# Performance work log

Hardware: AMD Instinct MI355X
Metric: run time of the kernel (lower is better)

## Reference

```python
import jax, jax.numpy as jnp
import numpy as np

N_NODES = 100000
N_EDGES = 640000
H_FEATS = 128


def setup_inputs() -> dict:
    key = jax.random.key(0)
    k_h, k_src, k_dst, k_w1, k_b1, k_w2, k_b2 = jax.random.split(key, 7)
    h = jax.random.normal(k_h, (N_NODES, H_FEATS), dtype=jnp.float32)
    src = jax.random.randint(k_src, (N_EDGES,), 0, N_NODES, dtype=jnp.int64)
    dst = jax.random.randint(k_dst, (N_EDGES,), 0, N_NODES, dtype=jnp.int64)
    # nn.Linear params: W1 (h_feats, 2*h_feats) as (out, in); store transposed for x @ W
    lim1 = 1.0 / np.sqrt(2 * H_FEATS)
    W1 = jax.random.uniform(k_w1, (2 * H_FEATS, H_FEATS), jnp.float32, -lim1, lim1)
    b1 = jax.random.uniform(k_b1, (H_FEATS,), jnp.float32, -lim1, lim1)
    lim2 = 1.0 / np.sqrt(H_FEATS)
    W2 = jax.random.uniform(k_w2, (H_FEATS, 1), jnp.float32, -lim2, lim2)
    b2 = jax.random.uniform(k_b2, (1,), jnp.float32, -lim2, lim2)
    return {"h": h, "src": src, "dst": dst, "W1": W1, "b1": b1, "W2": W2, "b2": b2}


def reference(h, src, dst, W1, b1, W2, b2):
    # gather src/dst node features per edge and concat: [E, 2*h_feats]
    he = jnp.concatenate([h[src], h[dst]], axis=1)
    hidden = jax.nn.relu(he @ W1 + b1)          # [E, h_feats]
    score = (hidden @ W2 + b2)[:, 0]            # [E]
    return score
```

## Files before the change

### kernel.cpp

```cpp
#include <hip/hip_runtime.h>

#define N_NODES 100000
#define N_EDGES 640000
#define F 128

typedef __attribute__((ext_vector_type(8))) short short8;
typedef __attribute__((ext_vector_type(4))) float float4v;

static __device__ __forceinline__ unsigned short f2bf(float f) {
    unsigned int u = __float_as_uint(f);
    u += 0x7fffu + ((u >> 16) & 1u);
    return (unsigned short)(u >> 16);
}

__global__ __launch_bounds__(256) void prep_wt(
    const float* __restrict__ W1, unsigned short* __restrict__ Wt)
{
    int id = blockIdx.x * 256 + threadIdx.x;
    int n = id >> 7, k = id & 127;
    float v = W1[((n & 128) + k) * 128 + (n & 127)];
    Wt[id] = f2bf(v);
}

__global__ __launch_bounds__(256) void node_proj(
    const float* __restrict__ h, const unsigned short* __restrict__ Wt,
    const float* __restrict__ b1,
    unsigned short* __restrict__ A, unsigned short* __restrict__ B)
{
    __shared__ unsigned short h_lds[64 * 136];
    __shared__ unsigned short w_lds[128 * 136];

    const int tid  = threadIdx.x;
    const int y    = blockIdx.y;
    const int node0 = blockIdx.x * 64;

#pragma unroll
    for (int i = 0; i < 8; ++i) {
        int idx = i * 256 + tid;
        int m = idx >> 5, c4 = idx & 31;
        int row_g = node0 + m; if (row_g >= N_NODES) row_g = N_NODES - 1;
        float4 v = *(const float4*)(h + (size_t)row_g * F + c4 * 4);
        uint2 p;
        p.x = (unsigned)f2bf(v.x) | ((unsigned)f2bf(v.y) << 16);
        p.y = (unsigned)f2bf(v.z) | ((unsigned)f2bf(v.w) << 16);
        *(uint2*)&h_lds[m * 136 + c4 * 4] = p;
    }
#pragma unroll
    for (int i = 0; i < 8; ++i) {
        int idx = i * 256 + tid;
        int n = idx >> 4, c = idx & 15;
        uint4 v = *(const uint4*)(Wt + (size_t)(y * 128 + n) * F + c * 8);
        *(uint4*)&w_lds[n * 136 + c * 8] = v;
    }
    __syncthreads();

    const int lane = tid & 63;
    const int l16  = lane & 15;
    const int quad = lane >> 4;
    const int w    = tid >> 6;
    const int n0w  = w * 32;
    const int kq   = quad * 8;

    float4v acc[4][2];
#pragma unroll
    for (int i = 0; i < 4; ++i)
#pragma unroll
        for (int j = 0; j < 2; ++j) acc[i][j] = (float4v){0.f, 0.f, 0.f, 0.f};

#pragma unroll
    for (int k0 = 0; k0 < 128; k0 += 32) {
        short8 af[4], bf[2];
#pragma unroll
        for (int i = 0; i < 4; ++i)
            af[i] = *(const short8*)&h_lds[(i * 16 + l16) * 136 + k0 + kq];
#pragma unroll
        for (int j = 0; j < 2; ++j)
            bf[j] = *(const short8*)&w_lds[(n0w + j * 16 + l16) * 136 + k0 + kq];
#pragma unroll
        for (int i = 0; i < 4; ++i)
#pragma unroll
            for (int j = 0; j < 2; ++j)
                acc[i][j] = __builtin_amdgcn_mfma_f32_16x16x32_bf16(
                    af[i], bf[j], acc[i][j], 0, 0, 0);
    }

    unsigned short* outp = (y == 0) ? A : B;
#pragma unroll
    for (int j = 0; j < 2; ++j) {
        int col = n0w + j * 16 + l16;
        float bias = (y == 0) ? b1[col] : 0.f;
#pragma unroll
        for (int i = 0; i < 4; ++i) {
#pragma unroll
            for (int r = 0; r < 4; ++r) {
                int row_g = node0 + i * 16 + quad * 4 + r;
                if (row_g < N_NODES)
                    outp[(size_t)row_g * F + col] = f2bf(acc[i][j][r] + bias);
            }
        }
    }
}

__global__ __launch_bounds__(256) void edge_score(
    const unsigned short* __restrict__ A, const unsigned short* __restrict__ B,
    const int* __restrict__ src, const int* __restrict__ dst,
    const float* __restrict__ W2, const float* __restrict__ b2,
    float* __restrict__ out)
{
    const int tid = threadIdx.x;
    const int sub = tid & 7;
    const int e   = blockIdx.x * 32 + (tid >> 3);
    const int j0  = sub * 16;

    const int s = src[e];
    const int d = dst[e];
    const uint4* Ap = (const uint4*)(A + (size_t)s * F + j0);
    const uint4* Bp = (const uint4*)(B + (size_t)d * F + j0);
    uint4 a0 = Ap[0], a1 = Ap[1];
    uint4 b0 = Bp[0], b1v = Bp[1];
    const float4* Wp = (const float4*)(W2 + j0);
    float4 w0 = Wp[0], w1 = Wp[1], w2 = Wp[2], w3 = Wp[3];

    float sacc = 0.f;
#define TERM(UA, UB, WL, WH)                                                   \
    {                                                                          \
        float fa0 = __uint_as_float((UA) << 16);                               \
        float fa1 = __uint_as_float((UA) & 0xFFFF0000u);                       \
        float fb0 = __uint_as_float((UB) << 16);                               \
        float fb1 = __uint_as_float((UB) & 0xFFFF0000u);                       \
        sacc = fmaf(fmaxf(fa0 + fb0, 0.f), (WL), sacc);                        \
        sacc = fmaf(fmaxf(fa1 + fb1, 0.f), (WH), sacc);                        \
    }
    TERM(a0.x, b0.x, w0.x, w0.y) TERM(a0.y, b0.y, w0.z, w0.w)
    TERM(a0.z, b0.z, w1.x, w1.y) TERM(a0.w, b0.w, w1.z, w1.w)
    TERM(a1.x, b1v.x, w2.x, w2.y) TERM(a1.y, b1v.y, w2.z, w2.w)
    TERM(a1.z, b1v.z, w3.x, w3.y) TERM(a1.w, b1v.w, w3.z, w3.w)
#undef TERM

    sacc += __shfl_xor(sacc, 1);
    sacc += __shfl_xor(sacc, 2);
    sacc += __shfl_xor(sacc, 4);

    if (sub == 0) out[e] = sacc + b2[0];
}

extern "C" void kernel_launch(void* const* d_in, const int* in_sizes, int n_in,
                              void* d_out, int out_size, void* d_ws, size_t ws_size,
                              hipStream_t stream) {
    const float* h   = (const float*)d_in[0];
    const int*   src = (const int*)d_in[1];
    const int*   dst = (const int*)d_in[2];
    const float* W1  = (const float*)d_in[3];
    const float* b1  = (const float*)d_in[4];
    const float* W2  = (const float*)d_in[5];
    const float* b2  = (const float*)d_in[6];
    float* out = (float*)d_out;

    unsigned short* Wt = (unsigned short*)d_ws;
    unsigned short* A  = Wt + 256 * 128;
    unsigned short* B  = A + (size_t)N_NODES * F;

    prep_wt<<<128, 256, 0, stream>>>(W1, Wt);
    node_proj<<<dim3((N_NODES + 63) / 64, 2), 256, 0, stream>>>(h, Wt, b1, A, B);
    edge_score<<<N_EDGES / 32, 256, 0, stream>>>(A, B, src, dst, W2, b2, out);
}
```

Measured before the change: 171.4 us.

## Load W fragments directly to registers and use one thread per edge

Measured after the change: 205.7 us. +20.0%, slower.

```diff
diff --git a/kernel.cpp b/kernel.cpp
--- a/kernel.cpp
+++ b/kernel.cpp
@@ -28,11 +28,25 @@
     unsigned short* __restrict__ A, unsigned short* __restrict__ B)
 {
     __shared__ unsigned short h_lds[64 * 136];
-    __shared__ unsigned short w_lds[128 * 136];
 
-    const int tid  = threadIdx.x;
-    const int y    = blockIdx.y;
+    const int tid   = threadIdx.x;
+    const int y     = blockIdx.y;
     const int node0 = blockIdx.x * 64;
+    const int lane  = tid & 63;
+    const int l16   = lane & 15;
+    const int quad  = lane >> 4;
+    const int w     = tid >> 6;
+    const int n0w   = w * 32;
+
+    short8 bfrag[2][4];
+#pragma unroll
+    for (int j = 0; j < 2; ++j) {
+        const unsigned short* wrow =
+            Wt + (size_t)(y * 128 + n0w + j * 16 + l16) * F + quad * 8;
+#pragma unroll
+        for (int k0 = 0; k0 < 4; ++k0)
+            bfrag[j][k0] = *(const short8*)(wrow + k0 * 32);
+    }
 
 #pragma unroll
     for (int i = 0; i < 8; ++i) {
@@ -45,21 +59,7 @@
         p.y = (unsigned)f2bf(v.z) | ((unsigned)f2bf(v.w) << 16);
         *(uint2*)&h_lds[m * 136 + c4 * 4] = p;
     }
-#pragma unroll
-    for (int i = 0; i < 8; ++i) {
-        int idx = i * 256 + tid;
-        int n = idx >> 4, c = idx & 15;
-        uint4 v = *(const uint4*)(Wt + (size_t)(y * 128 + n) * F + c * 8);
-        *(uint4*)&w_lds[n * 136 + c * 8] = v;
-    }
     __syncthreads();
-
-    const int lane = tid & 63;
-    const int l16  = lane & 15;
-    const int quad = lane >> 4;
-    const int w    = tid >> 6;
-    const int n0w  = w * 32;
-    const int kq   = quad * 8;
 
     float4v acc[4][2];
 #pragma unroll
@@ -68,20 +68,17 @@
         for (int j = 0; j < 2; ++j) acc[i][j] = (float4v){0.f, 0.f, 0.f, 0.f};
 
 #pragma unroll
-    for (int k0 = 0; k0 < 128; k0 += 32) {
-        short8 af[4], bf[2];
+    for (int k0 = 0; k0 < 4; ++k0) {
+        short8 af[4];
 #pragma unroll
         for (int i = 0; i < 4; ++i)
-            af[i] = *(const short8*)&h_lds[(i * 16 + l16) * 136 + k0 + kq];
-#pragma unroll
-        for (int j = 0; j < 2; ++j)
-            bf[j] = *(const short8*)&w_lds[(n0w + j * 16 + l16) * 136 + k0 + kq];
+            af[i] = *(const short8*)&h_lds[(i * 16 + l16) * 136 + k0 * 32 + quad * 8];
 #pragma unroll
         for (int i = 0; i < 4; ++i)
 #pragma unroll
             for (int j = 0; j < 2; ++j)
                 acc[i][j] = __builtin_amdgcn_mfma_f32_16x16x32_bf16(
-                    af[i], bf[j], acc[i][j], 0, 0, 0);
+                    af[i], bfrag[j][k0], acc[i][j], 0, 0, 0);
     }
 
     unsigned short* outp = (y == 0) ? A : B;
@@ -107,19 +104,11 @@
     const float* __restrict__ W2, const float* __restrict__ b2,
     float* __restrict__ out)
 {
-    const int tid = threadIdx.x;
-    const int sub = tid & 7;
-    const int e   = blockIdx.x * 32 + (tid >> 3);
-    const int j0  = sub * 16;
-
+    const int e = blockIdx.x * 256 + threadIdx.x;
     const int s = src[e];
     const int d = dst[e];
-    const uint4* Ap = (const uint4*)(A + (size_t)s * F + j0);
-    const uint4* Bp = (const uint4*)(B + (size_t)d * F + j0);
-    uint4 a0 = Ap[0], a1 = Ap[1];
-    uint4 b0 = Bp[0], b1v = Bp[1];
-    const float4* Wp = (const float4*)(W2 + j0);
-    float4 w0 = Wp[0], w1 = Wp[1], w2 = Wp[2], w3 = Wp[3];
+    const uint4* Ap = (const uint4*)(A + (size_t)s * F);
+    const uint4* Bp = (const uint4*)(B + (size_t)d * F);
 
     float sacc = 0.f;
 #define TERM(UA, UB, WL, WH)                                                   \
@@ -131,17 +120,20 @@
         sacc = fmaf(fmaxf(fa0 + fb0, 0.f), (WL), sacc);                        \
         sacc = fmaf(fmaxf(fa1 + fb1, 0.f), (WH), sacc);                        \
     }
-    TERM(a0.x, b0.x, w0.x, w0.y) TERM(a0.y, b0.y, w0.z, w0.w)
-    TERM(a0.z, b0.z, w1.x, w1.y) TERM(a0.w, b0.w, w1.z, w1.w)
-    TERM(a1.x, b1v.x, w2.x, w2.y) TERM(a1.y, b1v.y, w2.z, w2.w)
-    TERM(a1.z, b1v.z, w3.x, w3.y) TERM(a1.w, b1v.w, w3.z, w3.w)
+#pragma unroll
+    for (int c = 0; c < 16; ++c) {
+        uint4 av = Ap[c];
+        uint4 bv = Bp[c];
+        float4 wlo = ((const float4*)W2)[c * 2 + 0];
+        float4 whi = ((const float4*)W2)[c * 2 + 1];
+        TERM(av.x, bv.x, wlo.x, wlo.y)
+        TERM(av.y, bv.y, wlo.z, wlo.w)
+        TERM(av.z, bv.z, whi.x, whi.y)
+        TERM(av.w, bv.w, whi.z, whi.w)
+    }
 #undef TERM
 
-    sacc += __shfl_xor(sacc, 1);
-    sacc += __shfl_xor(sacc, 2);
-    sacc += __shfl_xor(sacc, 4);
-
-    if (sub == 0) out[e] = sacc + b2[0];
+    out[e] = sacc + b2[0];
 }
 
 extern "C" void kernel_launch(void* const* d_in, const int* in_sizes, int n_in,
@@ -162,5 +154,5 @@
 
     prep_wt<<<128, 256, 0, stream>>>(W1, Wt);
     node_proj<<<dim3((N_NODES + 63) / 64, 2), 256, 0, stream>>>(h, Wt, b1, A, B);
-    edge_score<<<N_EDGES / 32, 256, 0, stream>>>(A, B, src, dst, W2, b2, out);
+    edge_score<<<N_EDGES / 256, 256, 0, stream>>>(A, B, src, dst, W2, b2, out);
 }
```
